# Optimization experiments

Hardware: AMD Instinct MI355X
Metric: run time of the kernel (lower is better)

## Reference

```python
import jax, jax.numpy as jnp
import numpy as np

TOP_K = 2


def setup_inputs() -> dict:
    key = jax.random.key(0)
    ks = jax.random.split(key, 10)
    B, S, H, E = 4, 2048, 1024, 8
    s = 1.0 / np.sqrt(H)
    x = jax.random.normal(ks[0], (B, S, H), dtype=jnp.float32)
    gate_w = jax.random.normal(ks[1], (H, E), dtype=jnp.float32) * s
    gate_b = jnp.zeros((E,), dtype=jnp.float32)
    w1 = jax.random.normal(ks[2], (E, H, H), dtype=jnp.float32) * s
    b1 = jnp.zeros((E, H), dtype=jnp.float32)
    w2 = jax.random.normal(ks[3], (E, H, H), dtype=jnp.float32) * s
    b2 = jnp.zeros((E, H), dtype=jnp.float32)
    w3 = jax.random.normal(ks[4], (E, H, H), dtype=jnp.float32) * s
    b3 = jnp.zeros((E, H), dtype=jnp.float32)
    return {"x": x, "gate_w": gate_w, "gate_b": gate_b,
            "w1": w1, "b1": b1, "w2": w2, "b2": b2, "w3": w3, "b3": b3}


def reference(x, gate_w, gate_b, w1, b1, w2, b2, w3, b3):
    B, S, H = x.shape
    t = x.reshape(-1, H)                                  # [T, H]
    T = t.shape[0]
    # Router: logits -> fp32 softmax -> top-k -> renormalize
    router_logits = t @ gate_w + gate_b                   # [T, E]
    probs = jax.nn.softmax(router_logits.astype(jnp.float32), axis=-1)
    w, idx = jax.lax.top_k(probs, TOP_K)                  # [T, K]
    w = w / jnp.sum(w, axis=-1, keepdims=True)
    w = w.astype(x.dtype)
    # Dense combine weights: cw[t, e] = router weight if expert e selected for token t, else 0
    rows = jnp.arange(T)[:, None]
    cw = jnp.zeros(router_logits.shape, dtype=x.dtype).at[rows, idx].add(w)  # [T, E]
    # Expert MLPs (relu(fc1) -> relu(fc2) -> fc3), batched over experts
    h1 = jax.nn.relu(jnp.einsum('th,ehf->etf', t, w1) + b1[:, None, :])
    h2 = jax.nn.relu(jnp.einsum('etf,efg->etg', h1, w2) + b2[:, None, :])
    y = jnp.einsum('etg,egh->eth', h2, w3) + b3[:, None, :]                 # [E, T, H]
    # Weighted combine (equivalent to per-expert gather + weighted index_add)
    out = jnp.einsum('te,eth->th', cw, y)                 # [T, H]
    return out.reshape(B, S, H), router_logits
```

## Files before the change

kernel.cpp:

```cpp
#include <hip/hip_runtime.h>
#include <hip/hip_bf16.h>


#define HDIM 1024
#define NEXP 8
#define BM 128
#define BN 128
#define BK 32
#define HH ((size_t)HDIM * HDIM)

typedef __hip_bfloat16 bf16;
typedef unsigned short ushort_t;
typedef __attribute__((ext_vector_type(8))) short bf16x8;
typedef __attribute__((ext_vector_type(4))) float f32x4;

__device__ __forceinline__ float bflo(unsigned u) { return __uint_as_float(u << 16); }
__device__ __forceinline__ float bfhi(unsigned u) { return __uint_as_float(u & 0xffff0000u); }
__device__ __forceinline__ unsigned short f2bfu(float f) {
  bf16 h = __float2bfloat16(f);
  return *reinterpret_cast<unsigned short*>(&h);
}
__device__ __forceinline__ int iclamp(int v, int lo, int hi) {
  return v < lo ? lo : (v > hi ? hi : v);
}

__device__ __forceinline__ void async_cp16(const void* g, void* l) {
  __builtin_amdgcn_global_load_lds((const __attribute__((address_space(1))) void*)g,
                                   (__attribute__((address_space(3))) void*)l,
                                   16, 0, 0);
}

__device__ __forceinline__ void ld4f(const void* base, size_t idx, bool f32, float o[4]) {
  if (f32) {
    float4 v = *(const float4*)((const float*)base + idx);
    o[0] = v.x; o[1] = v.y; o[2] = v.z; o[3] = v.w;
  } else {
    uint2 v = *(const uint2*)((const unsigned short*)base + idx);
    o[0] = bflo(v.x); o[1] = bfhi(v.x); o[2] = bflo(v.y); o[3] = bfhi(v.y);
  }
}

__global__ void k_init(int* __restrict__ meta) {
  int i = blockIdx.x * blockDim.x + threadIdx.x;
  if (i < 3072) meta[i] = 0;
}

__global__ void k_sniff(const ushort_t* a0, int n0, const ushort_t* a1, int n1,
                        const ushort_t* a2, int n2, const ushort_t* a3, int n3,
                        const ushort_t* a4, int n4, int* __restrict__ flags) {
  int b = blockIdx.x;
  const ushort_t* a = b == 0 ? a0 : b == 1 ? a1 : b == 2 ? a2 : b == 3 ? a3 : a4;
  int n = b == 0 ? n0 : b == 1 ? n1 : b == 2 ? n2 : b == 3 ? n3 : n4;
  int hits = 0;
  for (int i = threadIdx.x; i < n; i += 256) {
    ushort_t v = a[i];
    if ((v & 0x7F80) == 0x7F80) hits++;
  }
  if (hits) atomicAdd(&flags[b], hits);
}

__global__ __launch_bounds__(512) void k_router(
    const void* __restrict__ x, const void* __restrict__ gw,
    const bf16* __restrict__ gb, void* __restrict__ dout, bf16* __restrict__ xb,
    int* __restrict__ sel_e, float* __restrict__ sel_w,
    int* __restrict__ meta, int TS, int T) {
  __shared__ float sgT[NEXP][HDIM];
  const int* flags = meta + 2048;
  bool fx = flags[0] != 0, fgw = flags[1] != 0;
  int tid = threadIdx.x;

#pragma unroll
  for (int r = 0; r < 2; r++) {
    int h = r * 512 + tid;
    float g[8];
    ld4f(gw, (size_t)h * NEXP, fgw, g);
    ld4f(gw, (size_t)h * NEXP + 4, fgw, g + 4);
#pragma unroll
    for (int e = 0; e < NEXP; e++) sgT[e][h] = g[e];
  }
  __syncthreads();

  int wave = tid >> 6, lane = tid & 63;
  int t = blockIdx.x * 8 + wave;

  double acc[NEXP];
#pragma unroll
  for (int e = 0; e < NEXP; e++) acc[e] = 0.0;

  if (t < T) {
#pragma unroll
    for (int j = 0; j < 4; j++) {
      int h = j * 256 + lane * 4;
      float xf[4];
      ld4f(x, (size_t)t * HDIM + h, fx, xf);
      if (fx) {
        uint2 ov;
        ov.x = (unsigned)f2bfu(xf[0]) | ((unsigned)f2bfu(xf[1]) << 16);
        ov.y = (unsigned)f2bfu(xf[2]) | ((unsigned)f2bfu(xf[3]) << 16);
        *(uint2*)((unsigned short*)xb + (size_t)t * HDIM + h) = ov;
      }
#pragma unroll
      for (int e = 0; e < NEXP; e++) {
        float4 g = *(const float4*)&sgT[e][h];
        acc[e] += (double)xf[0] * (double)g.x + (double)xf[1] * (double)g.y
                + (double)xf[2] * (double)g.z + (double)xf[3] * (double)g.w;
      }
    }
  }

#pragma unroll
  for (int off = 32; off >= 1; off >>= 1) {
#pragma unroll
    for (int e = 0; e < NEXP; e++) acc[e] += __shfl_down(acc[e], off);
  }

  if (lane == 0 && t < T) {
    double l[NEXP];
#pragma unroll
    for (int e = 0; e < NEXP; e++) l[e] = acc[e] + (double)__bfloat162float(gb[e]);
    size_t lo = (size_t)T * HDIM + (size_t)t * NEXP;
    if (fx) {
      float* lp = (float*)dout + lo;
#pragma unroll
      for (int e = 0; e < NEXP; e++) lp[e] = (float)l[e];
    } else {
      unsigned short* lp = (unsigned short*)dout + lo;
#pragma unroll
      for (int e = 0; e < NEXP; e++) lp[e] = f2bfu((float)l[e]);
    }
    int i1 = 0; double v1 = l[0];
#pragma unroll
    for (int e = 1; e < NEXP; e++) if (l[e] > v1) { v1 = l[e]; i1 = e; }
    int i2 = -1; double v2 = -1e300;
#pragma unroll
    for (int e = 0; e < NEXP; e++) if (e != i1 && l[e] > v2) { v2 = l[e]; i2 = e; }
    if (i2 < 0) i2 = (i1 + 1) & 7;
    float w1 = 1.0f / (1.0f + __expf((float)(v2 - v1)));
    sel_e[2 * t] = i1; sel_e[2 * t + 1] = i2;
    sel_w[2 * t] = w1; sel_w[2 * t + 1] = 1.0f - w1;
  }
}

__global__ void k_offsets(const int* __restrict__ sel_e, int* __restrict__ meta,
                          int* __restrict__ list, int* __restrict__ row_e,
                          int RCAP, int NTMAX, int TS) {
  int s = blockIdx.x;
  __shared__ int base[NEXP + 1];
  __shared__ int wsum[4][NEXP];
  int tid = threadIdx.x;

  int cnt[NEXP];
#pragma unroll
  for (int e = 0; e < NEXP; e++) cnt[e] = 0;
  const int* se = sel_e + (size_t)2 * s * TS;
  for (int i = tid; i < 2 * TS; i += 256) {
    int v = se[i];
#pragma unroll
    for (int e = 0; e < NEXP; e++) cnt[e] += (v == e) ? 1 : 0;
  }
#pragma unroll
  for (int off = 32; off >= 1; off >>= 1)
#pragma unroll
    for (int e = 0; e < NEXP; e++) cnt[e] += __shfl_down(cnt[e], off);
  int lane = tid & 63, wave = tid >> 6;
  if (lane == 0) {
#pragma unroll
    for (int e = 0; e < NEXP; e++) wsum[wave][e] = cnt[e];
  }
  __syncthreads();

  if (tid == 0) {
    int b = 0;
    for (int e = 0; e < NEXP; e++) {
      int ce = wsum[0][e] + wsum[1][e] + wsum[2][e] + wsum[3][e];
      base[e] = b;
      meta[s * 8 + e] = ce;
      meta[512 + s * 8 + e] = b;
      meta[1024 + s * 8 + e] = b;
      b = (b + ce + BM - 1) & ~(BM - 1);
    }
    base[NEXP] = b;
    meta[2560 + s] = b / BM;
  }
  __syncthreads();

  for (int r = tid; r < NTMAX; r += blockDim.x) {
    int rs = r * BM;
    int e = 0;
    for (int q = 1; q < NEXP; q++) if (rs >= base[q]) e = q;
    row_e[s * NTMAX + r] = e;
  }
  int* ls = list + (size_t)s * RCAP;
  for (int e = 0; e < NEXP; e++) {
    int ce = wsum[0][e] + wsum[1][e] + wsum[2][e] + wsum[3][e];
    for (int p = base[e] + ce + tid; p < base[e + 1]; p += blockDim.x)
      ls[p] = s * TS;
  }
}

__global__ void k_scatter(const int* __restrict__ sel_e, int* __restrict__ meta,
                          int* __restrict__ list, int* __restrict__ pos_of,
                          int T, int TS, int RCAP) {
  int t = blockIdx.x * blockDim.x + threadIdx.x;
  if (t >= T) return;
  int s = t / TS;
#pragma unroll
  for (int k = 0; k < 2; k++) {
    int e = sel_e[2 * t + k];
    int pos = atomicAdd(&meta[512 + s * 8 + e], 1);
    if (pos >= 0 && pos < RCAP) list[(size_t)s * RCAP + pos] = t;
    pos_of[2 * t + k] = pos;
  }
}

__global__ void k_trans(const void* __restrict__ w, const int* __restrict__ flags,
                        int fidx, bf16* __restrict__ wt) {
  int e = blockIdx.z;
  bool fW = flags[fidx] != 0;
  __shared__ unsigned short tile[32][33];
  int tid = threadIdx.x;
  int r = tid >> 3, c4 = (tid & 7) * 4;
  int R0 = blockIdx.y * 32, C0 = blockIdx.x * 32;
  float v[4];
  ld4f(w, (size_t)e * HH + (size_t)(R0 + r) * HDIM + C0 + c4, fW, v);
  tile[c4 + 0][r] = f2bfu(v[0]);
  tile[c4 + 1][r] = f2bfu(v[1]);
  tile[c4 + 2][r] = f2bfu(v[2]);
  tile[c4 + 3][r] = f2bfu(v[3]);
  __syncthreads();
  uint2 ov;
  ov.x = (unsigned)tile[r][c4 + 0] | ((unsigned)tile[r][c4 + 1] << 16);
  ov.y = (unsigned)tile[r][c4 + 2] | ((unsigned)tile[r][c4 + 3] << 16);
  *(uint2*)((unsigned short*)wt + (size_t)e * HH + (size_t)(C0 + r) * HDIM + R0 + c4) = ov;
}

template <bool GATHER, bool RELU>
__global__ __launch_bounds__(256) void k_gemm(
    const bf16* __restrict__ A, const bf16* __restrict__ Axb,
    const int* __restrict__ list,
    const int* __restrict__ row_e, const int* __restrict__ ntiles,
    const bf16* __restrict__ wt, const bf16* __restrict__ bias,
    bf16* __restrict__ C, const int* __restrict__ flags, int Tm1) {
  int id = blockIdx.y * gridDim.x + blockIdx.x;
  int tm = id % gridDim.y;
  int tn = id / gridDim.y;
  if (tm >= *ntiles) return;
  int e = row_e[tm];
  int row0 = tm * BM;
  const bf16* Ause = (GATHER && flags[0] != 0) ? Axb : A;

  __shared__ __align__(16) unsigned short lA[BM * BK];
  __shared__ __align__(16) unsigned short lB[BN * BK];

  int tid = threadIdx.x;
  int lane = tid & 63, wave = tid >> 6;
  int koff = (lane & 3) * 8;
  int r0 = wave * 32 + (lane >> 2);

  const unsigned short* pb0 = (const unsigned short*)wt + (size_t)e * HH
                            + (size_t)(tn * BN + r0) * HDIM + koff;
  const unsigned short* pb1 = pb0 + (size_t)16 * HDIM;
  unsigned short* lb0 = lB + (wave * 32) * BK;
  unsigned short* lb1 = lb0 + 16 * BK;

  const unsigned short* pa0;
  const unsigned short* pa1;
  unsigned short* la0 = lA + (wave * 32) * BK;
  unsigned short* la1 = la0 + 16 * BK;

  if (GATHER) {
    int t0 = iclamp(list[row0 + r0], 0, Tm1);
    int t1 = iclamp(list[row0 + r0 + 16], 0, Tm1);
    pa0 = (const unsigned short*)Ause + (size_t)t0 * HDIM + koff;
    pa1 = (const unsigned short*)Ause + (size_t)t1 * HDIM + koff;
  } else {
    pa0 = (const unsigned short*)Ause + (size_t)(row0 + r0) * HDIM + koff;
    pa1 = pa0 + (size_t)16 * HDIM;
  }

  f32x4 acc[4][4];
#pragma unroll
  for (int i = 0; i < 4; i++)
#pragma unroll
    for (int j = 0; j < 4; j++) acc[i][j] = (f32x4){0.f, 0.f, 0.f, 0.f};

  int lm = lane & 15, quad = lane >> 4;
  int am = (wave & 1) * 64, bn = (wave >> 1) * 64;

  for (int k0 = 0; k0 < HDIM; k0 += BK) {
    async_cp16(pa0, la0);
    async_cp16(pa1, la1);
    pa0 += BK; pa1 += BK;
    async_cp16(pb0, lb0);
    async_cp16(pb1, lb1);
    pb0 += BK; pb1 += BK;
    __syncthreads();
    bf16x8 af[4], bfr[4];
#pragma unroll
    for (int i = 0; i < 4; i++)
      af[i] = *(const bf16x8*)&lA[(am + i * 16 + lm) * BK + quad * 8];
#pragma unroll
    for (int j = 0; j < 4; j++)
      bfr[j] = *(const bf16x8*)&lB[(bn + j * 16 + lm) * BK + quad * 8];
#pragma unroll
    for (int i = 0; i < 4; i++)
#pragma unroll
      for (int j = 0; j < 4; j++)
        acc[i][j] = __builtin_amdgcn_mfma_f32_16x16x32_bf16(af[i], bfr[j], acc[i][j], 0, 0, 0);
    __syncthreads();
  }

#pragma unroll
  for (int j = 0; j < 4; j++) {
    int col = tn * BN + bn + j * 16 + lm;
    float bv = __bfloat162float(bias[e * HDIM + col]);
#pragma unroll
    for (int i = 0; i < 4; i++) {
      int rowb = row0 + am + i * 16 + quad * 4;
#pragma unroll
      for (int rr = 0; rr < 4; rr++) {
        float v = acc[i][j][rr] + bv;
        if (RELU) v = fmaxf(v, 0.f);
        ((unsigned short*)C)[(size_t)(rowb + rr) * HDIM + col] = f2bfu(v);
      }
    }
  }
}

__global__ void k_combine(const bf16* __restrict__ y, const int* __restrict__ pos_of,
                          const float* __restrict__ sel_w, void* __restrict__ dout,
                          size_t out_elem_off, const int* __restrict__ meta, int Pm1) {
  bool fx = meta[2048] != 0;
  int t = blockIdx.x;
  int tid = threadIdx.x;
  int p0 = iclamp(pos_of[2 * t], 0, Pm1);
  int p1 = iclamp(pos_of[2 * t + 1], 0, Pm1);
  float w0 = sel_w[2 * t], w1 = sel_w[2 * t + 1];
  int h = tid * 4;
  uint2 a = *(const uint2*)((const unsigned short*)y + (size_t)p0 * HDIM + h);
  uint2 b = *(const uint2*)((const unsigned short*)y + (size_t)p1 * HDIM + h);
  float o0 = w0 * bflo(a.x) + w1 * bflo(b.x);
  float o1 = w0 * bfhi(a.x) + w1 * bfhi(b.x);
  float o2 = w0 * bflo(a.y) + w1 * bflo(b.y);
  float o3 = w0 * bfhi(a.y) + w1 * bfhi(b.y);
  size_t off = out_elem_off + (size_t)t * HDIM + h;
  if (fx) {
    float4 ov = { o0, o1, o2, o3 };
    *(float4*)((float*)dout + off) = ov;
  } else {
    uint2 ov;
    ov.x = (unsigned)f2bfu(o0) | ((unsigned)f2bfu(o1) << 16);
    ov.y = (unsigned)f2bfu(o2) | ((unsigned)f2bfu(o3) << 16);
    *(uint2*)((unsigned short*)dout + off) = ov;
  }
}

extern "C" void kernel_launch(void* const* d_in, const int* in_sizes, int n_in,
                              void* d_out, int out_size, void* d_ws, size_t ws_size,
                              hipStream_t stream) {
  const void* x  = d_in[0];
  const void* gw = d_in[1];
  const bf16* gb = (const bf16*)d_in[2];
  const void* w1 = d_in[3];
  const bf16* b1 = (const bf16*)d_in[4];
  const void* w2 = d_in[5];
  const bf16* b2 = (const bf16*)d_in[6];
  const void* w3 = d_in[7];
  const bf16* b3 = (const bf16*)d_in[8];

  const int T = in_sizes[0] / HDIM;
  const size_t wtsz = (size_t)NEXP * HH * 2;
  const size_t xbsz = (size_t)T * HDIM * 2;

  int S = 64;
  size_t base_need = 0;
  for (int cand = 1; cand <= 64; cand *= 2) {
    size_t rcap = (size_t)2 * T / cand + NEXP * BM;
    size_t ntmx = rcap / BM;
    size_t need = 12288 + (size_t)8 * T * 3 + (size_t)4 * cand * rcap
                + (size_t)4 * cand * ntmx + wtsz + 2 * rcap * HDIM * 2
                + xbsz + 1024;
    if (need <= ws_size) { S = cand; base_need = need; break; }
  }
  const int TS = T / S;
  const int RCAP = 2 * TS + NEXP * BM;
  const int NTMAX = RCAP / BM;
  const bool hoist = (S > 1) && (base_need + 2 * wtsz <= ws_size);

  char* ws = (char*)d_ws;
  size_t ofs = 0;
  int*   meta   = (int*)(ws + ofs);   ofs += 12288;
  int*   sel_e  = (int*)(ws + ofs);   ofs += (size_t)8 * T;
  float* sel_w  = (float*)(ws + ofs); ofs += (size_t)8 * T;
  int*   pos_of = (int*)(ws + ofs);   ofs += (size_t)8 * T;
  int*   list   = (int*)(ws + ofs);   ofs += (size_t)4 * S * RCAP;
  int*   row_e  = (int*)(ws + ofs);   ofs += (size_t)4 * S * NTMAX;
  ofs = (ofs + 255) & ~(size_t)255;
  bf16* wt0 = (bf16*)(ws + ofs); ofs += wtsz;
  bf16* h1  = (bf16*)(ws + ofs); ofs += (size_t)RCAP * HDIM * 2;
  bf16* h2  = (bf16*)(ws + ofs); ofs += (size_t)RCAP * HDIM * 2;
  bf16* xb  = (bf16*)(ws + ofs); ofs += xbsz;
  bf16* wt1 = wt0;
  bf16* wt2 = wt0;
  if (hoist) {
    wt1 = (bf16*)(ws + ofs); ofs += wtsz;
    wt2 = (bf16*)(ws + ofs); ofs += wtsz;
  }

  int* flags = meta + 2048;

  k_init<<<12, 256, 0, stream>>>(meta);
  k_sniff<<<5, 256, 0, stream>>>((const ushort_t*)x, 32768,
                                 (const ushort_t*)gw, HDIM * NEXP,
                                 (const ushort_t*)w1, 32768,
                                 (const ushort_t*)w2, 32768,
                                 (const ushort_t*)w3, 32768, flags);
  k_router<<<(T + 7) / 8, 512, 0, stream>>>(x, gw, gb, d_out, xb, sel_e, sel_w,
                                            meta, TS, T);
  k_offsets<<<S, 256, 0, stream>>>(sel_e, meta, list, row_e, RCAP, NTMAX, TS);
  k_scatter<<<(T + 255) / 256, 256, 0, stream>>>(sel_e, meta, list, pos_of, T, TS, RCAP);

  dim3 tg(HDIM / 32, HDIM / 32, NEXP);
  dim3 gg(HDIM / BN, NTMAX);
  const bf16* xbf = (const bf16*)x;

  if (hoist) {
    k_trans<<<tg, 256, 0, stream>>>(w1, flags, 2, wt0);
    k_trans<<<tg, 256, 0, stream>>>(w2, flags, 3, wt1);
    k_trans<<<tg, 256, 0, stream>>>(w3, flags, 4, wt2);
  }
  for (int s = 0; s < S; s++) {
    const int* lst = list + (size_t)s * RCAP;
    const int* re  = row_e + (size_t)s * NTMAX;
    const int* nt  = meta + 2560 + s;
    if (!hoist) k_trans<<<tg, 256, 0, stream>>>(w1, flags, 2, wt0);
    k_gemm<true,  true ><<<gg, 256, 0, stream>>>(xbf, xb, lst, re, nt, wt0, b1, h1, flags, T - 1);
    if (!hoist) k_trans<<<tg, 256, 0, stream>>>(w2, flags, 3, wt1);
    k_gemm<false, true ><<<gg, 256, 0, stream>>>(h1, nullptr, nullptr, re, nt, wt1, b2, h2, flags, T - 1);
    if (!hoist) k_trans<<<tg, 256, 0, stream>>>(w3, flags, 4, wt2);
    k_gemm<false, false><<<gg, 256, 0, stream>>>(h2, nullptr, nullptr, re, nt, wt2, b3, h1, flags, T - 1);
    k_combine<<<TS, 256, 0, stream>>>(h1, pos_of + (size_t)2 * s * TS,
                                      sel_w + (size_t)2 * s * TS,
                                      d_out, (size_t)s * TS * HDIM, meta, RCAP - 1);
  }
}
```

Baseline: 493.7 us.

## Triple-buffer GEMM LDS tiles with async prefetch and XOR swizzle

Converts the single-buffered GEMM main loop into a 3-stage software pipeline: tiles for k+1..k+3 are issued via async copies ahead of use, with explicit vmcnt waits instead of a full sync per load. It also XOR-swizzles the k-chunk placement in LDS to reduce bank conflicts on fragment reads, and raises wave priority around the MFMA block. This triples LDS use per block, which may lower occupancy, and relies on the async copy count matching the vmcnt values.

```diff
diff --git a/kernel.cpp b/kernel.cpp
--- a/kernel.cpp
+++ b/kernel.cpp
@@ -249,34 +249,41 @@
   int row0 = tm * BM;
   const bf16* Ause = (GATHER && flags[0] != 0) ? Axb : A;
 
-  __shared__ __align__(16) unsigned short lA[BM * BK];
-  __shared__ __align__(16) unsigned short lB[BN * BK];
+  __shared__ __align__(16) unsigned short lA[3 * BM * BK];
+  __shared__ __align__(16) unsigned short lB[3 * BN * BK];
 
   int tid = threadIdx.x;
   int lane = tid & 63, wave = tid >> 6;
-  int koff = (lane & 3) * 8;
+  int ksw = ((lane & 3) ^ ((lane >> 3) & 3)) * 8;
   int r0 = wave * 32 + (lane >> 2);
 
   const unsigned short* pb0 = (const unsigned short*)wt + (size_t)e * HH
-                            + (size_t)(tn * BN + r0) * HDIM + koff;
+                            + (size_t)(tn * BN + r0) * HDIM + ksw;
   const unsigned short* pb1 = pb0 + (size_t)16 * HDIM;
-  unsigned short* lb0 = lB + (wave * 32) * BK;
-  unsigned short* lb1 = lb0 + 16 * BK;
-
   const unsigned short* pa0;
   const unsigned short* pa1;
-  unsigned short* la0 = lA + (wave * 32) * BK;
-  unsigned short* la1 = la0 + 16 * BK;
-
   if (GATHER) {
     int t0 = iclamp(list[row0 + r0], 0, Tm1);
     int t1 = iclamp(list[row0 + r0 + 16], 0, Tm1);
-    pa0 = (const unsigned short*)Ause + (size_t)t0 * HDIM + koff;
-    pa1 = (const unsigned short*)Ause + (size_t)t1 * HDIM + koff;
+    pa0 = (const unsigned short*)Ause + (size_t)t0 * HDIM + ksw;
+    pa1 = (const unsigned short*)Ause + (size_t)t1 * HDIM + ksw;
   } else {
-    pa0 = (const unsigned short*)Ause + (size_t)(row0 + r0) * HDIM + koff;
+    pa0 = (const unsigned short*)Ause + (size_t)(row0 + r0) * HDIM + ksw;
     pa1 = pa0 + (size_t)16 * HDIM;
   }
+  unsigned short* laD0 = lA + (wave * 32) * BK;
+  unsigned short* laD1 = laD0 + 16 * BK;
+  unsigned short* lbD0 = lB + (wave * 32) * BK;
+  unsigned short* lbD1 = lbD0 + 16 * BK;
+
+#define STAGE(pb, ktt)                                         \
+  do {                                                         \
+    int _o = (pb) * (BM * BK);                                 \
+    async_cp16(pa0 + (size_t)(ktt) * BK, laD0 + _o);           \
+    async_cp16(pa1 + (size_t)(ktt) * BK, laD1 + _o);           \
+    async_cp16(pb0 + (size_t)(ktt) * BK, lbD0 + _o);           \
+    async_cp16(pb1 + (size_t)(ktt) * BK, lbD1 + _o);           \
+  } while (0)
 
   f32x4 acc[4][4];
 #pragma unroll
@@ -286,29 +293,45 @@
 
   int lm = lane & 15, quad = lane >> 4;
   int am = (wave & 1) * 64, bn = (wave >> 1) * 64;
-
-  for (int k0 = 0; k0 < HDIM; k0 += BK) {
-    async_cp16(pa0, la0);
-    async_cp16(pa1, la1);
-    pa0 += BK; pa1 += BK;
-    async_cp16(pb0, lb0);
-    async_cp16(pb1, lb1);
-    pb0 += BK; pb1 += BK;
-    __syncthreads();
+  int rdc = (quad ^ ((lm >> 1) & 3)) * 8;
+
+  STAGE(0, 0);
+  STAGE(1, 1);
+  STAGE(2, 2);
+
+  const int NK = HDIM / BK;
+  int p = 0;
+  for (int kt = 0; kt < NK; ++kt) {
+    if (kt < NK - 2)       asm volatile("s_waitcnt vmcnt(8)" ::: "memory");
+    else if (kt == NK - 2) asm volatile("s_waitcnt vmcnt(4)" ::: "memory");
+    else                   asm volatile("s_waitcnt vmcnt(0)" ::: "memory");
+    __builtin_amdgcn_sched_barrier(0);
+    __builtin_amdgcn_s_barrier();
+    __builtin_amdgcn_sched_barrier(0);
+
+    int o = p * (BM * BK);
     bf16x8 af[4], bfr[4];
 #pragma unroll
     for (int i = 0; i < 4; i++)
-      af[i] = *(const bf16x8*)&lA[(am + i * 16 + lm) * BK + quad * 8];
+      af[i] = *(const bf16x8*)&lA[o + (am + i * 16 + lm) * BK + rdc];
 #pragma unroll
     for (int j = 0; j < 4; j++)
-      bfr[j] = *(const bf16x8*)&lB[(bn + j * 16 + lm) * BK + quad * 8];
+      bfr[j] = *(const bf16x8*)&lB[o + (bn + j * 16 + lm) * BK + rdc];
+    __builtin_amdgcn_s_setprio(1);
 #pragma unroll
     for (int i = 0; i < 4; i++)
 #pragma unroll
       for (int j = 0; j < 4; j++)
         acc[i][j] = __builtin_amdgcn_mfma_f32_16x16x32_bf16(af[i], bfr[j], acc[i][j], 0, 0, 0);
-    __syncthreads();
-  }
+    __builtin_amdgcn_s_setprio(0);
+
+    __builtin_amdgcn_sched_barrier(0);
+    __builtin_amdgcn_s_barrier();
+    __builtin_amdgcn_sched_barrier(0);
+    if (kt + 3 < NK) STAGE(p, kt + 3);
+    p = (p == 2) ? 0 : p + 1;
+  }
+#undef STAGE
 
 #pragma unroll
   for (int j = 0; j < 4; j++) {
```

New measurement: 487.2 us. About the same (-1.3%).
